# Kernel tuning notes

Measured on AMD Instinct MI355X. Metric: run time of the kernel, lower is better.

The kernel has to match this reference:

```python
import jax, jax.numpy as jnp
import numpy as np

ALPHA = 0.05   # propalpha
GDEP = 2       # gcn_depth
DIL = 2        # new_dilation
KSET = (2, 3, 6, 7)

def _dconv(x, w, b, d):
    # Conv2d(c_in, c_out, (1, k), dilation=(1, d), padding='same'), NCHW layout
    k = w.shape[-1]
    tot = d * (k - 1)
    lo = tot // 2
    y = jax.lax.conv_general_dilated(x, w, (1, 1), ((0, 0), (lo, tot - lo)),
                                     rhs_dilation=(1, d),
                                     dimension_numbers=('NCHW', 'OIHW', 'NCHW'))
    return y + b[None, :, None, None]

def _inception(x, ws, bs):
    # 'same' padding keeps seq_len for every branch, so the tail-slice is a no-op
    return jnp.concatenate([_dconv(x, w, b, DIL) for w, b in zip(ws, bs)], axis=1)

def _gcn(Hf, Aoff, W, b, n):
    # PyG GCNConv with unit edge weights (no edge_weight passed) and remaining self-loops:
    # out = D^-1/2 (A_off + I_R)^T D^-1/2 (Hf @ W^T) + b, where only rows < n carry edges.
    XW = Hf @ W.T
    deg = jnp.ones((Hf.shape[0],), Hf.dtype).at[:n].add(jnp.sum(Aoff, axis=0))
    dis = jax.lax.rsqrt(deg)
    out = XW / deg[:, None]                                           # self-loop term
    out = out.at[:n].add(dis[:n, None] * (Aoff.T @ (dis[:n, None] * XW[:n])))
    return out + b[None, :]

def _mixprop(X, A, gws, gbs, mw, mb):
    B, C, n, L = X.shape
    # dense_to_sparse ignores weights here (none passed to GCNConv) -> binary adjacency;
    # add_remaining_self_loops replaces any diagonal entries, so zero the diagonal.
    Aoff = (A != 0).astype(X.dtype) * (1.0 - jnp.eye(n, dtype=X.dtype))
    H = X
    hops = [X]
    for i in range(GDEP):
        Hf = H.reshape(B * L, C * n)   # torch row-major reshape, replicated exactly
        H1 = _gcn(Hf, Aoff, gws[i], gbs[i], n)
        H = ALPHA * X + H1.reshape(B, C, n, L)
        hops.append(H)
    Hc = jnp.concatenate(hops, axis=1)  # (B, (GDEP+1)*C, n, L)
    return jnp.einsum('bixl,oi->boxl', Hc, mw) + mb[None, :, None, None]

def _layernorm(x, w, b, idx, eps=1e-5):
    # F.layer_norm over all of x.shape[1:] with node-indexed affine params
    mu = jnp.mean(x, axis=(1, 2, 3), keepdims=True)
    var = jnp.var(x, axis=(1, 2, 3), keepdims=True)
    xh = (x - mu) * jax.lax.rsqrt(var + eps)
    return xh * w[:, idx, :][None] + b[:, idx, :][None]

def _forward(x, x_skip, A, idx, fws, fbs, gws, gbs, skip_w, skip_b,
             mp1_gw, mp1_gb, mp1_mw, mp1_mb, mp2_gw, mp2_gb, mp2_mw, mp2_mb,
             ln_w, ln_b):
    x_res = x
    xf = jnp.tanh(_inception(x, fws, fbs))
    xg = jax.nn.sigmoid(_inception(x, gws, gbs))
    x = xf * xg  # gated dilated temporal conv (dropout is an eval-mode no-op)
    x_skip = jnp.einsum('bixl,oi->boxl', x, skip_w) + skip_b[None, :, None, None] + x_skip
    x = (_mixprop(x, A, mp1_gw, mp1_gb, mp1_mw, mp1_mb)
         + _mixprop(x.swapaxes(0, 0), A.T, mp2_gw, mp2_gb, mp2_mw, mp2_mb))
    x = x + x_res[..., -x.shape[3]:]
    x = _layernorm(x, ln_w, ln_b, idx)
    return x, x_skip

def setup_inputs():
    key = jax.random.key(0)
    ks = jax.random.split(key, 32)
    B, C, N, L, SKIP = 16, 32, 128, 128, 64
    F = C * N
    co = C // len(KSET)
    d = {}
    d['x'] = jax.random.normal(ks[0], (B, C, N, L), jnp.float32)
    d['x_skip'] = jax.random.normal(ks[1], (B, SKIP, N, L), jnp.float32)
    d['A'] = jax.random.uniform(ks[2], (N, N), jnp.float32)
    d['idx'] = jnp.arange(N, dtype=jnp.int32)
    i = 3
    for pre in ('f', 'g'):
        for k in KSET:
            d[pre + 'w' + str(k)] = jax.random.normal(ks[i], (co, C, 1, k), jnp.float32) * float(1.0 / np.sqrt(C * k))
            d[pre + 'b' + str(k)] = jax.random.uniform(ks[i + 1], (co,), jnp.float32)
            i += 2
    d['skip_w'] = jax.random.normal(ks[i], (SKIP, C), jnp.float32) * float(1.0 / np.sqrt(C)); i += 1
    d['skip_b'] = jax.random.uniform(ks[i], (SKIP,), jnp.float32); i += 1
    for mp in ('mp1', 'mp2'):
        d[mp + '_gw'] = jax.random.normal(ks[i], (GDEP, F, F), jnp.float32) * float(1.0 / np.sqrt(F)); i += 1
        d[mp + '_gb'] = jnp.zeros((GDEP, F), jnp.float32)
        d[mp + '_mw'] = jax.random.normal(ks[i], (C, (GDEP + 1) * C), jnp.float32) * float(1.0 / np.sqrt((GDEP + 1) * C)); i += 1
        d[mp + '_mb'] = jax.random.uniform(ks[i], (C,), jnp.float32); i += 1
    d['ln_w'] = jnp.ones((C, N, L), jnp.float32)
    d['ln_b'] = jnp.zeros((C, N, L), jnp.float32)
    return d

def reference(x, x_skip, A, idx, fw2, fb2, fw3, fb3, fw6, fb6, fw7, fb7,
              gw2, gb2, gw3, gb3, gw6, gb6, gw7, gb7, skip_w, skip_b,
              mp1_gw, mp1_gb, mp1_mw, mp1_mb, mp2_gw, mp2_gb, mp2_mw, mp2_mb,
              ln_w, ln_b):
    return _forward(x, x_skip, A, idx,
                    [fw2, fw3, fw6, fw7], [fb2, fb3, fb6, fb7],
                    [gw2, gw3, gw6, gw7], [gb2, gb3, gb6, gb7],
                    skip_w, skip_b, mp1_gw, mp1_gb, mp1_mw, mp1_mb,
                    mp2_gw, mp2_gb, mp2_mw, mp2_mb, ln_w, ln_b)
```

## Files before the change

kernel.cpp:

```cpp
#include <hip/hip_runtime.h>
#include <stdint.h>

typedef unsigned short u16;
typedef unsigned int   u32;
typedef __attribute__((ext_vector_type(4))) float f32x4;
typedef __attribute__((ext_vector_type(8))) short bf16x8;

__device__ __forceinline__ u16 f2bf(float f) {
    u32 i = __float_as_uint(f);
    u32 r = (i + 0x7fffu + ((i >> 16) & 1u)) >> 16;
    return (u16)r;
}
__device__ __forceinline__ float bf2f(u16 u) {
    return __uint_as_float(((u32)u) << 16);
}
__device__ __forceinline__ u32 cvt2bf(float a, float b) {
    u32 r;
    asm("v_cvt_pk_bf16_f32 %0, %1, %2" : "=v"(r) : "v"(a), "v"(b));
    return r;
}

#define GLOAD16(g, l) __builtin_amdgcn_global_load_lds( \
    (const __attribute__((address_space(1))) void*)(g), \
    (__attribute__((address_space(3))) void*)(l), 16, 0, 0)

#define RAW_BARRIER()  asm volatile("s_barrier" ::: "memory")
#define VMCNT(n)       asm volatile("s_waitcnt vmcnt(" #n ")" ::: "memory")

__global__ __launch_bounds__(512, 1)
void k_gemm2g(const u16* __restrict__ A0, const u16* __restrict__ A1,
              const u16* __restrict__ B0, const u16* __restrict__ B1,
              const u16* __restrict__ Gres,
              const float* __restrict__ gb0, const float* __restrict__ gb1,
              u16* __restrict__ Ha, u16* __restrict__ Hb,
              float* __restrict__ XW0a, float* __restrict__ XW0b)
{
    __shared__ alignas(16) u16 LDS[65536];
    const int NT = 128;
    const int tid  = threadIdx.x;
    const int lane = tid & 63;
    const int wid  = tid >> 6;
    const int wr = wid >> 2, wc = wid & 3;

    const int bid = blockIdx.x;
    const int swz = (bid & 7) * 32 + (bid >> 3);
    const int z   = swz >> 7;
    const int rem = swz & 127;
    const int bm = (rem >> 4) * 256;
    const int bn = (rem & 15) * 256;

    const u16* Ap = (z ? A1 : A0) + (size_t)bm * 4096;
    const u16* Bp = (z ? B1 : B0) + (size_t)bn * 4096;

    int aoff[8], boff[4];
    #pragma unroll
    for (int i = 0; i < 8; ++i) {
        int row = wr * 128 + i * 16 + (lane & 15);
        int sp  = (lane >> 4) ^ ((row >> 1) & 3);
        aoff[i] = row * 32 + sp * 8;
    }
    #pragma unroll
    for (int j = 0; j < 4; ++j) {
        int row = wc * 64 + j * 16 + (lane & 15);
        int sp  = (lane >> 4) ^ ((row >> 1) & 3);
        boff[j] = row * 32 + sp * 8;
    }

    auto stage = [&](int t) {
        if (t >= NT) return;
        const int k0  = t << 5;
        u16* buf = LDS + ((t & 3) << 14);
        #pragma unroll
        for (int h = 0; h < 2; ++h) {
            const int c  = tid + h * 512;
            const int r  = c >> 2;
            const int sl = (c & 3) ^ ((r >> 1) & 3);
            GLOAD16(Ap + (size_t)r * 4096 + k0 + sl * 8, buf + c * 8);
            GLOAD16(Bp + (size_t)r * 4096 + k0 + sl * 8, buf + 8192 + c * 8);
        }
    };

    f32x4 acc[8][4] = {};

    auto compute = [&](int t) {
        const u16* buf = LDS + ((t & 3) << 14);
        bf16x8 af[8], bf[4];
        #pragma unroll
        for (int j = 0; j < 4; ++j) bf[j] = *(const bf16x8*)(buf + 8192 + boff[j]);
        #pragma unroll
        for (int i = 0; i < 8; ++i) af[i] = *(const bf16x8*)(buf + aoff[i]);
        __builtin_amdgcn_s_setprio(1);
        #pragma unroll
        for (int i = 0; i < 8; ++i)
            #pragma unroll
            for (int j = 0; j < 4; ++j)
                acc[i][j] = __builtin_amdgcn_mfma_f32_16x16x32_bf16(af[i], bf[j], acc[i][j], 0, 0, 0);
        __builtin_amdgcn_s_setprio(0);
    };

    stage(0); stage(1); stage(2);
    for (int t = 0; t < NT - 3; ++t) {
        VMCNT(8);
        RAW_BARRIER();
        stage(t + 3);
        compute(t);
    }
    VMCNT(8);  RAW_BARRIER(); compute(NT - 3);
    VMCNT(4);  RAW_BARRIER(); compute(NT - 2);
    VMCNT(0);  RAW_BARRIER(); compute(NT - 1);

    const int orow = (lane >> 4) * 4, ocol = lane & 15;
    const float* gbv = z ? gb1 : gb0;
    u16* H = z ? Hb : Ha;

    #pragma unroll
    for (int j = 0; j < 4; ++j) {
        const int o = bn + wc * 64 + j * 16 + ocol;
        const float gbo = gbv[o];
        #pragma unroll
        for (int i = 0; i < 8; ++i) {
            const int rbase = bm + wr * 128 + i * 16 + orow;
            #pragma unroll
            for (int v = 0; v < 4; ++v) {
                const size_t e = (size_t)(rbase + v) * 4096 + o;
                float g = bf2f(Gres[e]);
                H[e] = f2bf(__fmaf_rn(0.05f, g, acc[i][j][v] + gbo));
            }
        }
    }
    if (bm == 0 && wr == 0) {
        float* XW0 = z ? XW0b : XW0a;
        #pragma unroll
        for (int i = 0; i < 8; ++i) {
            #pragma unroll
            for (int j = 0; j < 4; ++j) {
                float* cp = XW0 + (size_t)(i * 16 + orow) * 4096 + (bn + wc * 64 + j * 16 + ocol);
                #pragma unroll
                for (int v = 0; v < 4; ++v)
                    cp[(size_t)v * 4096] = acc[i][j][v];
            }
        }
    }
}

__device__ __forceinline__ void wcvt_body(int wb, const float* __restrict__ W0,
                                          const float* __restrict__ W1,
                                          u16* __restrict__ Wb0, u16* __restrict__ Wb1)
{
    int half = wb >> 13;
    const float* W = half ? W1 : W0;
    u16* Wb = half ? Wb1 : Wb0;
    size_t e = ((size_t)(wb & 8191) * 256 + threadIdx.x) * 8;
    f32x4 a = *(const f32x4*)(W + e);
    f32x4 b = *(const f32x4*)(W + e + 4);
    uint4 r;
    r.x = cvt2bf(a[0], a[1]); r.y = cvt2bf(a[2], a[3]);
    r.z = cvt2bf(b[0], b[1]); r.w = cvt2bf(b[2], b[3]);
    *(uint4*)(Wb + e) = r;
}

__device__ __forceinline__ void prep_body(const float* __restrict__ A, float* dd)
{
    int r = threadIdx.x;
    if (r >= 128) return;
    int cc = 0, cr = 0;
    for (int j = 0; j < 128; ++j) {
        if (j == r) continue;
        if (A[(j << 7) + r] != 0.f) cc++;
        if (A[(r << 7) + j] != 0.f) cr++;
    }
    float d1 = 1.f + (float)cc, d2 = 1.f + (float)cr;
    dd[r]       = rsqrtf(d1); dd[128 + r] = 1.f / d1;
    dd[256 + r] = rsqrtf(d2); dd[384 + r] = 1.f / d2;
}

__device__ __forceinline__ void gcnfix_body(int fb, const float* __restrict__ XW0a,
              const float* __restrict__ XW0b,
              const u16* __restrict__ G, const float* __restrict__ Af,
              const float* __restrict__ dd,
              const float* __restrict__ gb0, const float* __restrict__ gb1,
              u16* __restrict__ Ha, u16* __restrict__ Hb)
{
    const int prob = fb >> 9;
    const int rem  = fb & 511;
    const int t4 = rem * 256 + threadIdx.x;
    const int r = t4 >> 10, og = (t4 & 1023) << 2;
    const float* XW0 = prob ? XW0b : XW0a;
    const float* dis = prob ? dd + 256 : dd;
    const float* inv = prob ? dd + 384 : dd + 128;
    const float* gb  = prob ? gb1  : gb0;
    u16* H = prob ? Hb : Ha;

    const size_t e = ((size_t)r << 12) + og;
    f32x4 xw = *(const f32x4*)(XW0 + e);
    f32x4 s = {0.f, 0.f, 0.f, 0.f};
    for (int j = 0; j < 128; ++j) {
        float av = prob ? Af[(r << 7) + j] : Af[(j << 7) + r];
        float wv = ((av != 0.f) && (j != r)) ? dis[j] : 0.f;
        f32x4 xv = *(const f32x4*)(XW0 + ((size_t)j << 12) + og);
        #pragma unroll
        for (int q = 0; q < 4; ++q) s[q] = __fmaf_rn(wv, xv[q], s[q]);
    }
    const float iv = inv[r], dr = dis[r];
    f32x4 gb4 = *(const f32x4*)(gb + og);
    uint2 gv = *(const uint2*)(G + e);
    float g0 = __uint_as_float(gv.x << 16), g1 = __uint_as_float(gv.x & 0xffff0000u);
    float g2 = __uint_as_float(gv.y << 16), g3 = __uint_as_float(gv.y & 0xffff0000u);
    float y0 = __fmaf_rn(0.05f, g0, __fmaf_rn(dr, s[0], xw[0] * iv) + gb4[0]);
    float y1 = __fmaf_rn(0.05f, g1, __fmaf_rn(dr, s[1], xw[1] * iv) + gb4[1]);
    float y2 = __fmaf_rn(0.05f, g2, __fmaf_rn(dr, s[2], xw[2] * iv) + gb4[2]);
    float y3 = __fmaf_rn(0.05f, g3, __fmaf_rn(dr, s[3], xw[3] * iv) + gb4[3]);
    uint2 rr;
    rr.x = cvt2bf(y0, y1);
    rr.y = cvt2bf(y2, y3);
    *(uint2*)(H + e) = rr;
}

__device__ __forceinline__ constexpr int wbase_of(int k) {
    return k == 2 ? 0 : k == 3 ? 520 : k == 6 ? 1296 : 2840;
}
__device__ __forceinline__ constexpr int ob_of(int k) {
    return k == 2 ? 0 : k == 3 ? 8 : k == 6 ? 16 : 24;
}

template<int KA, int KB>
__device__ __forceinline__ void conv_dual(const float* __restrict__ xsb,
                                          const float* __restrict__ wfA,
                                          const float* __restrict__ wgA,
                                          const float* __restrict__ wfB,
                                          const float* __restrict__ wgB,
                                          float fbA, float gbA, float fbB, float gbB,
                                          u16* __restrict__ GpA, u16* __restrict__ GpB,
                                          u16* __restrict__ GsA, u16* __restrict__ GsB)
{
    float afA[8], agA[8], afB[8], agB[8];
    #pragma unroll
    for (int i = 0; i < 8; ++i) {
        afA[i] = fbA; agA[i] = gbA;
        afB[i] = fbB; agB[i] = gbB;
    }
    for (int c = 0; c < 32; ++c) {
        float xw[24];
        const float* xr = xsb + c * 144;
        #pragma unroll
        for (int q = 0; q < 6; ++q) {
            f32x4 v = *(const f32x4*)(xr + q * 4);
            xw[q * 4 + 0] = v[0]; xw[q * 4 + 1] = v[1];
            xw[q * 4 + 2] = v[2]; xw[q * 4 + 3] = v[3];
        }
        {
            float wf[KA], wg[KA];
            const float* pf = wfA + c * KA;
            const float* pg = wgA + c * KA;
            #pragma unroll
            for (int j = 0; j < KA; ++j) { wf[j] = pf[j]; wg[j] = pg[j]; }
            #pragma unroll
            for (int li = 0; li < 8; ++li) {
                #pragma unroll
                for (int j = 0; j < KA; ++j) {
                    float xv = xw[li + 8 - (KA - 1) + 2 * j];
                    afA[li] = __fmaf_rn(xv, wf[j], afA[li]);
                    agA[li] = __fmaf_rn(xv, wg[j], agA[li]);
                }
            }
        }
        {
            float wf[KB], wg[KB];
            const float* pf = wfB + c * KB;
            const float* pg = wgB + c * KB;
            #pragma unroll
            for (int j = 0; j < KB; ++j) { wf[j] = pf[j]; wg[j] = pg[j]; }
            #pragma unroll
            for (int li = 0; li < 8; ++li) {
                #pragma unroll
                for (int j = 0; j < KB; ++j) {
                    float xv = xw[li + 8 - (KB - 1) + 2 * j];
                    afB[li] = __fmaf_rn(xv, wf[j], afB[li]);
                    agB[li] = __fmaf_rn(xv, wg[j], agB[li]);
                }
            }
        }
    }
    u16 oA[8], oB[8];
    #pragma unroll
    for (int i = 0; i < 8; ++i) {
        float e2 = __expf(2.f * afA[i]);
        float th = 1.f - __fdividef(2.f, e2 + 1.f);
        float sg = __fdividef(1.f, 1.f + __expf(-agA[i]));
        oA[i] = f2bf(th * sg);
        float e2b = __expf(2.f * afB[i]);
        float thb = 1.f - __fdividef(2.f, e2b + 1.f);
        float sgb = __fdividef(1.f, 1.f + __expf(-agB[i]));
        oB[i] = f2bf(thb * sgb);
    }
    uint4 uA, uB;
    uA.x = oA[0] | ((u32)oA[1] << 16); uA.y = oA[2] | ((u32)oA[3] << 16);
    uA.z = oA[4] | ((u32)oA[5] << 16); uA.w = oA[6] | ((u32)oA[7] << 16);
    uB.x = oB[0] | ((u32)oB[1] << 16); uB.y = oB[2] | ((u32)oB[3] << 16);
    uB.z = oB[4] | ((u32)oB[5] << 16); uB.w = oB[6] | ((u32)oB[7] << 16);
    *(uint4*)GpA = uA; *(uint4*)GpB = uB;
    *(uint4*)GsA = uA; *(uint4*)GsB = uB;
}

__global__ __launch_bounds__(256)
void k_mega1(const float* __restrict__ x,
             const float* __restrict__ fw2p, const float* __restrict__ fw3p,
             const float* __restrict__ fw6p, const float* __restrict__ fw7p,
             const float* __restrict__ fb2p, const float* __restrict__ fb3p,
             const float* __restrict__ fb6p, const float* __restrict__ fb7p,
             const float* __restrict__ gw2p, const float* __restrict__ gw3p,
             const float* __restrict__ gw6p, const float* __restrict__ gw7p,
             const float* __restrict__ gb2p, const float* __restrict__ gb3p,
             const float* __restrict__ gb6p, const float* __restrict__ gb7p,
             const float* __restrict__ sw,   const float* __restrict__ sb,
             const float* __restrict__ xskip,
             u16* __restrict__ G, float* __restrict__ outp,
             const float* __restrict__ W0, const float* __restrict__ W1,
             u16* __restrict__ Wb0, u16* __restrict__ Wb1,
             const float* __restrict__ A, float* __restrict__ dd)
{
    const int bid = blockIdx.x;
    if (bid >= 2048) {
        if (bid < 18432) wcvt_body(bid - 2048, W0, W1, Wb0, Wb1);
        else             prep_body(A, dd);
        return;
    }
    __shared__ alignas(16) float xs[32 * 144];
    __shared__ float wfl[4640], wgl[4640];
    __shared__ float fbl[32], gbl[32];
    __shared__ alignas(16) u16 Gs[4096];
    __shared__ float swl[64 * 33];
    __shared__ float sbl[64];
    const int tid = threadIdx.x;
    const int b = bid >> 7, n = bid & 127;

    for (int i = tid; i < 32 * 144; i += 256) xs[i] = 0.f;
    for (int g = tid; g < 4608; g += 256) {
        int rel, k, woff;
        const float *pf, *pg;
        if (g < 512)       { rel = g;        k = 2; woff = 0;    pf = fw2p; pg = gw2p; }
        else if (g < 1280) { rel = g - 512;  k = 3; woff = 520;  pf = fw3p; pg = gw3p; }
        else if (g < 2816) { rel = g - 1280; k = 6; woff = 1296; pf = fw6p; pg = gw6p; }
        else               { rel = g - 2816; k = 7; woff = 2840; pf = fw7p; pg = gw7p; }
        int ck = 32 * k;
        int oo = rel / ck, rem = rel % ck;
        int dst = woff + oo * (ck + 1) + rem;
        wfl[dst] = pf[rel];
        wgl[dst] = pg[rel];
    }
    for (int i = tid; i < 2048; i += 256) swl[(i >> 5) * 33 + (i & 31)] = sw[i];
    if (tid < 64) sbl[tid] = sb[tid];
    if (tid < 32) {
        int br = tid >> 3, oo = tid & 7;
        const float* pf = br == 0 ? fb2p : br == 1 ? fb3p : br == 2 ? fb6p : fb7p;
        const float* pg = br == 0 ? gb2p : br == 1 ? gb3p : br == 2 ? gb6p : gb7p;
        fbl[tid] = pf[oo]; gbl[tid] = pg[oo];
    }
    __syncthreads();
    const float* xb = x + (size_t)b * 524288 + n * 128;
    for (int p = 0; p < 4; ++p) {
        int chunk = p * 256 + tid;
        int c = chunk >> 5, l4 = (chunk & 31) * 4;
        *(f32x4*)&xs[c * 144 + 8 + l4] = *(const f32x4*)(xb + (size_t)c * 16384 + l4);
    }
    __syncthreads();

    {
        const int w = tid >> 6, lane = tid & 63;
        const int oo = lane >> 3, lL = lane & 7;
        const int h  = w & 1;
        const int l0 = h * 64 + lL * 8;
        const float* xsb = xs + l0;
        size_t gbase = ((size_t)b * 32 * 128 + n) * 128 + l0;
        if (w < 2) {
            constexpr int KA = 2, KB = 7;
            const int oA = ob_of(KA) + oo, oB = ob_of(KB) + oo;
            conv_dual<KA, KB>(xsb,
                wfl + wbase_of(KA) + oo * (32 * KA + 1), wgl + wbase_of(KA) + oo * (32 * KA + 1),
                wfl + wbase_of(KB) + oo * (32 * KB + 1), wgl + wbase_of(KB) + oo * (32 * KB + 1),
                fbl[oA], gbl[oA], fbl[oB], gbl[oB],
                G + gbase + (size_t)oA * 16384, G + gbase + (size_t)oB * 16384,
                Gs + oA * 128 + l0, Gs + oB * 128 + l0);
        } else {
            constexpr int KA = 3, KB = 6;
            const int oA = ob_of(KA) + oo, oB = ob_of(KB) + oo;
            conv_dual<KA, KB>(xsb,
                wfl + wbase_of(KA) + oo * (32 * KA + 1), wgl + wbase_of(KA) + oo * (32 * KA + 1),
                wfl + wbase_of(KB) + oo * (32 * KB + 1), wgl + wbase_of(KB) + oo * (32 * KB + 1),
                fbl[oA], gbl[oA], fbl[oB], gbl[oB],
                G + gbase + (size_t)oA * 16384, G + gbase + (size_t)oB * 16384,
                Gs + oA * 128 + l0, Gs + oB * 128 + l0);
        }
    }
    __syncthreads();

    const int sg = (tid & 15) * 4, l0s = (tid >> 4) * 8;
    float acc[4][8];
    #pragma unroll
    for (int si = 0; si < 4; ++si) {
        float bv = sbl[sg + si];
        #pragma unroll
        for (int li = 0; li < 8; ++li) acc[si][li] = bv;
    }
    for (int c = 0; c < 32; ++c) {
        uint4 gv = *(const uint4*)&Gs[c * 128 + l0s];
        float g[8];
        g[0] = __uint_as_float(gv.x << 16); g[1] = __uint_as_float(gv.x & 0xffff0000u);
        g[2] = __uint_as_float(gv.y << 16); g[3] = __uint_as_float(gv.y & 0xffff0000u);
        g[4] = __uint_as_float(gv.z << 16); g[5] = __uint_as_float(gv.z & 0xffff0000u);
        g[6] = __uint_as_float(gv.w << 16); g[7] = __uint_as_float(gv.w & 0xffff0000u);
        #pragma unroll
        for (int si = 0; si < 4; ++si) {
            float wv = swl[(sg + si) * 33 + c];
            #pragma unroll
            for (int li = 0; li < 8; ++li) acc[si][li] = __fmaf_rn(g[li], wv, acc[si][li]);
        }
    }
    #pragma unroll
    for (int si = 0; si < 4; ++si) {
        size_t e = ((size_t)(b * 64 + sg + si) * 128 + n) * 128 + l0s;
        f32x4 x0 = *(const f32x4*)(xskip + e);
        f32x4 x1 = *(const f32x4*)(xskip + e + 4);
        f32x4 r0, r1;
        r0[0] = acc[si][0] + x0[0]; r0[1] = acc[si][1] + x0[1];
        r0[2] = acc[si][2] + x0[2]; r0[3] = acc[si][3] + x0[3];
        r1[0] = acc[si][4] + x1[0]; r1[1] = acc[si][5] + x1[1];
        r1[2] = acc[si][6] + x1[2]; r1[3] = acc[si][7] + x1[3];
        *(f32x4*)(outp + e)     = r0;
        *(f32x4*)(outp + e + 4) = r1;
    }
}

__global__ __launch_bounds__(256)
void k_mega2(const float* __restrict__ XW0a, const float* __restrict__ XW0b,
             const u16* __restrict__ G, const float* __restrict__ Af,
             const float* __restrict__ dd,
             const float* __restrict__ gb0, const float* __restrict__ gb1,
             u16* __restrict__ Ha, u16* __restrict__ Hb,
             const float* __restrict__ W0, const float* __restrict__ W1,
             u16* __restrict__ Wb0, u16* __restrict__ Wb1)
{
    const int bid = blockIdx.x;
    if (bid < 1024) gcnfix_body(bid, XW0a, XW0b, G, Af, dd, gb0, gb1, Ha, Hb);
    else            wcvt_body(bid - 1024, W0, W1, Wb0, Wb1);
}

__global__ __launch_bounds__(256)
void k_gcnfix(const float* __restrict__ XW0a, const float* __restrict__ XW0b,
              const u16* __restrict__ G, const float* __restrict__ Af,
              const float* __restrict__ dd,
              const float* __restrict__ gb0, const float* __restrict__ gb1,
              u16* __restrict__ Ha, u16* __restrict__ Hb)
{
    gcnfix_body(blockIdx.x, XW0a, XW0b, G, Af, dd, gb0, gb1, Ha, Hb);
}

__global__ __launch_bounds__(256)
void k_mix2ln(const u16* __restrict__ G,
              const u16* __restrict__ H1, const u16* __restrict__ H2,
              const u16* __restrict__ H1b, const u16* __restrict__ H2b,
              const float* __restrict__ mw1, const float* __restrict__ mb1,
              const float* __restrict__ mw2, const float* __restrict__ mb2,
              const float* __restrict__ x,
              u16* __restrict__ Y, float* __restrict__ partial)
{
    __shared__ alignas(16) u16 Gs[4096], H1s[4096], H2s[4096], H1bs[4096], H2bs[4096];
    __shared__ float wSg[32 * 33], wS11[32 * 33], wS12[32 * 33], wS21[32 * 33], wS22[32 * 33];
    __shared__ float mbl[32];
    const int tid = threadIdx.x;
    const int b = blockIdx.x >> 7, xn = blockIdx.x & 127;
    size_t base = (size_t)b * 524288 + xn * 128;
    for (int p = 0; p < 2; ++p) {
        int chunk = p * 256 + tid, c = chunk >> 4, l8 = (chunk & 15) * 8;
        size_t src = base + (size_t)c * 16384 + l8;
        *(uint4*)&Gs[c * 128 + l8]   = *(const uint4*)(G + src);
        *(uint4*)&H1s[c * 128 + l8]  = *(const uint4*)(H1 + src);
        *(uint4*)&H2s[c * 128 + l8]  = *(const uint4*)(H2 + src);
        *(uint4*)&H1bs[c * 128 + l8] = *(const uint4*)(H1b + src);
        *(uint4*)&H2bs[c * 128 + l8] = *(const uint4*)(H2b + src);
    }
    for (int i = tid; i < 1024; i += 256) {
        int o = i >> 5, c = i & 31;
        int d = o * 33 + c;
        wSg[d]  = mw1[o * 96 + c] + mw2[o * 96 + c];
        wS11[d] = mw1[o * 96 + 32 + c];
        wS12[d] = mw1[o * 96 + 64 + c];
        wS21[d] = mw2[o * 96 + 32 + c];
        wS22[d] = mw2[o * 96 + 64 + c];
    }
    if (tid < 32) mbl[tid] = mb1[tid] + mb2[tid];
    __syncthreads();
    const int og = (tid & 7) * 4, l0 = (tid >> 3) * 4;
    float acc[4][4];
    #pragma unroll
    for (int oi = 0; oi < 4; ++oi) {
        float bv = mbl[og + oi];
        acc[oi][0] = bv; acc[oi][1] = bv; acc[oi][2] = bv; acc[oi][3] = bv;
    }
    for (int c = 0; c < 32; ++c) {
        uint2 ga = *(const uint2*)&Gs[c * 128 + l0];
        uint2 h1 = *(const uint2*)&H1s[c * 128 + l0];
        uint2 h2 = *(const uint2*)&H2s[c * 128 + l0];
        uint2 j1 = *(const uint2*)&H1bs[c * 128 + l0];
        uint2 j2 = *(const uint2*)&H2bs[c * 128 + l0];
        float gv[4], v1[4], v2[4], u1[4], u2[4];
        gv[0] = __uint_as_float(ga.x << 16); gv[1] = __uint_as_float(ga.x & 0xffff0000u);
        gv[2] = __uint_as_float(ga.y << 16); gv[3] = __uint_as_float(ga.y & 0xffff0000u);
        v1[0] = __uint_as_float(h1.x << 16); v1[1] = __uint_as_float(h1.x & 0xffff0000u);
        v1[2] = __uint_as_float(h1.y << 16); v1[3] = __uint_as_float(h1.y & 0xffff0000u);
        v2[0] = __uint_as_float(h2.x << 16); v2[1] = __uint_as_float(h2.x & 0xffff0000u);
        v2[2] = __uint_as_float(h2.y << 16); v2[3] = __uint_as_float(h2.y & 0xffff0000u);
        u1[0] = __uint_as_float(j1.x << 16); u1[1] = __uint_as_float(j1.x & 0xffff0000u);
        u1[2] = __uint_as_float(j1.y << 16); u1[3] = __uint_as_float(j1.y & 0xffff0000u);
        u2[0] = __uint_as_float(j2.x << 16); u2[1] = __uint_as_float(j2.x & 0xffff0000u);
        u2[2] = __uint_as_float(j2.y << 16); u2[3] = __uint_as_float(j2.y & 0xffff0000u);
        #pragma unroll
        for (int oi = 0; oi < 4; ++oi) {
            int d = (og + oi) * 33 + c;
            float a0 = wSg[d], a1 = wS11[d], a2 = wS12[d], a3 = wS21[d], a4 = wS22[d];
            #pragma unroll
            for (int li = 0; li < 4; ++li)
                acc[oi][li] += gv[li] * a0 + v1[li] * a1 + v2[li] * a2
                             + u1[li] * a3 + u2[li] * a4;
        }
    }
    float s = 0.f, ss = 0.f;
    #pragma unroll
    for (int oi = 0; oi < 4; ++oi) {
        size_t e = ((size_t)(b * 32 + og + oi) * 128 + xn) * 128 + l0;
        f32x4 xv = *(const f32x4*)(x + e);
        float y0 = acc[oi][0] + xv[0];
        float y1 = acc[oi][1] + xv[1];
        float y2 = acc[oi][2] + xv[2];
        float y3 = acc[oi][3] + xv[3];
        s  += y0 + y1 + y2 + y3;
        ss += y0 * y0 + y1 * y1 + y2 * y2 + y3 * y3;
        uint2 rr;
        rr.x = cvt2bf(y0, y1);
        rr.y = cvt2bf(y2, y3);
        *(uint2*)(Y + e) = rr;
    }
    #pragma unroll
    for (int o = 32; o > 0; o >>= 1) {
        s  += __shfl_down(s,  o, 64);
        ss += __shfl_down(ss, o, 64);
    }
    __shared__ float sred[8];
    int w = tid >> 6;
    if ((tid & 63) == 0) { sred[w * 2] = s; sred[w * 2 + 1] = ss; }
    __syncthreads();
    if (tid == 0) {
        partial[blockIdx.x * 2]     = sred[0] + sred[2] + sred[4] + sred[6];
        partial[blockIdx.x * 2 + 1] = sred[1] + sred[3] + sred[5] + sred[7];
    }
}

__global__ __launch_bounds__(256)
void k_lnnorm(const u16* __restrict__ Y,
              const float* __restrict__ partial, const int* __restrict__ idxp,
              const float* __restrict__ lnw, const float* __restrict__ lnb,
              float* __restrict__ outx)
{
    const int tid = threadIdx.x;
    const int b = blockIdx.x >> 7, chunk = blockIdx.x & 127;
    float s = 0.f, ss = 0.f;
    if (tid < 128) {
        s  = partial[(b * 128 + tid) * 2];
        ss = partial[(b * 128 + tid) * 2 + 1];
    }
    #pragma unroll
    for (int o = 32; o > 0; o >>= 1) {
        s  += __shfl_down(s,  o, 64);
        ss += __shfl_down(ss, o, 64);
    }
    __shared__ float sred[4];
    __shared__ float mv[2];
    if ((tid & 63) == 0 && tid < 128) { sred[(tid >> 6) * 2] = s; sred[(tid >> 6) * 2 + 1] = ss; }
    __syncthreads();
    if (tid == 0) {
        float S = sred[0] + sred[2], SS = sred[1] + sred[3];
        float mean = S * (1.f / 524288.f);
        float var = SS * (1.f / 524288.f) - mean * mean;
        mv[0] = mean; mv[1] = rsqrtf(var + 1e-5f);
    }
    __syncthreads();
    const float mean = mv[0], rstd = mv[1];
    #pragma unroll
    for (int q = 0; q < 4; ++q) {
        int ib = chunk * 4096 + q * 1024 + tid * 4;
        size_t e = (size_t)b * 524288 + ib;
        uint2 yv2 = *(const uint2*)(Y + e);
        float y[4];
        y[0] = __uint_as_float(yv2.x << 16); y[1] = __uint_as_float(yv2.x & 0xffff0000u);
        y[2] = __uint_as_float(yv2.y << 16); y[3] = __uint_as_float(yv2.y & 0xffff0000u);
        int c = ib >> 14, xn = (ib >> 7) & 127, l = ib & 127;
        int ix = idxp[xn];
        size_t we = ((size_t)c * 128 + ix) * 128 + l;
        f32x4 wv = *(const f32x4*)(lnw + we);
        f32x4 bv = *(const f32x4*)(lnb + we);
        f32x4 r;
        #pragma unroll
        for (int j = 0; j < 4; ++j)
            r[j] = (y[j] - mean) * rstd * wv[j] + bv[j];
        *(f32x4*)(outx + e) = r;
    }
}

extern "C" void kernel_launch(void* const* d_in, const int* in_sizes, int n_in,
                              void* d_out, int out_size, void* d_ws, size_t ws_size,
                              hipStream_t stream)
{
    (void)in_sizes; (void)n_in; (void)out_size; (void)ws_size;
    const float* x      = (const float*)d_in[0];
    const float* xskip  = (const float*)d_in[1];
    const float* A      = (const float*)d_in[2];
    const int*   idxp   = (const int*)d_in[3];
    const float* fw2p = (const float*)d_in[4];  const float* fb2p = (const float*)d_in[5];
    const float* fw3p = (const float*)d_in[6];  const float* fb3p = (const float*)d_in[7];
    const float* fw6p = (const float*)d_in[8];  const float* fb6p = (const float*)d_in[9];
    const float* fw7p = (const float*)d_in[10]; const float* fb7p = (const float*)d_in[11];
    const float* gw2p = (const float*)d_in[12]; const float* gb2p = (const float*)d_in[13];
    const float* gw3p = (const float*)d_in[14]; const float* gb3p = (const float*)d_in[15];
    const float* gw6p = (const float*)d_in[16]; const float* gb6p = (const float*)d_in[17];
    const float* gw7p = (const float*)d_in[18]; const float* gb7p = (const float*)d_in[19];
    const float* sw   = (const float*)d_in[20]; const float* sb   = (const float*)d_in[21];
    const float* mp1_gw = (const float*)d_in[22]; const float* mp1_gb = (const float*)d_in[23];
    const float* mp1_mw = (const float*)d_in[24]; const float* mp1_mb = (const float*)d_in[25];
    const float* mp2_gw = (const float*)d_in[26]; const float* mp2_gb = (const float*)d_in[27];
    const float* mp2_mw = (const float*)d_in[28]; const float* mp2_mb = (const float*)d_in[29];
    const float* lnw = (const float*)d_in[30]; const float* lnb = (const float*)d_in[31];

    char* wsb = (char*)d_ws;
    float* out_x  = (float*)d_out;
    float* out_sk = out_x + 8388608;

    const size_t MB16 = 16777216, MB33 = 33554432;
    u16*   G    = (u16*)(wsb);
    u16*   H1   = (u16*)(wsb + MB16);
    u16*   H1b  = (u16*)(wsb + 2 * MB16);
    u16*   H2   = (u16*)(wsb + 3 * MB16);
    u16*   H2b  = (u16*)(wsb + 4 * MB16);
    u16*   Wb0  = (u16*)(wsb + 5 * MB16);
    u16*   Wb1  = (u16*)(wsb + 5 * MB16 + MB33);
    u16*   Yb   = (u16*)Wb0;
    float* XW0a = (float*)(wsb + 5 * MB16 + 2 * MB33);
    float* XW0b = (float*)(wsb + 5 * MB16 + 2 * MB33 + 2097152);
    float* part = (float*)(wsb + 5 * MB16 + 2 * MB33 + 4194304);
    float* dd   = (float*)(wsb + 5 * MB16 + 2 * MB33 + 4194304 + 16384);

    k_mega1<<<18433, 256, 0, stream>>>(x, fw2p, fw3p, fw6p, fw7p, fb2p, fb3p, fb6p, fb7p,
                                       gw2p, gw3p, gw6p, gw7p, gb2p, gb3p, gb6p, gb7p,
                                       sw, sb, xskip, G, out_sk,
                                       mp1_gw, mp2_gw, Wb0, Wb1, A, dd);
    k_gemm2g<<<256, 512, 0, stream>>>(G, G, Wb0, Wb1, G, mp1_gb, mp2_gb,
                                      H1, H1b, XW0a, XW0b);
    k_mega2<<<17408, 256, 0, stream>>>(XW0a, XW0b, G, A, dd, mp1_gb, mp2_gb,
                                       H1, H1b, mp1_gw + MB16, mp2_gw + MB16, Wb0, Wb1);
    k_gemm2g<<<256, 512, 0, stream>>>(H1, H1b, Wb0, Wb1, G, mp1_gb + 4096, mp2_gb + 4096,
                                      H2, H2b, XW0a, XW0b);
    k_gcnfix<<<1024, 256, 0, stream>>>(XW0a, XW0b, G, A, dd,
                                       mp1_gb + 4096, mp2_gb + 4096, H2, H2b);
    k_mix2ln<<<2048, 256, 0, stream>>>(G, H1, H2, H1b, H2b, mp1_mw, mp1_mb,
                                       mp2_mw, mp2_mb, x, Yb, part);
    k_lnnorm<<<2048, 256, 0, stream>>>(Yb, part, idxp, lnw, lnb, out_x);
}
```

Measured before the change: 644.0 us.

## Split inception from weight-convert kernel and store conv weights as bf16 in LDS

The fused mega1 kernel is split into a standalone weight-conversion/prep kernel and a dedicated inception+skip kernel. Inside the inception kernel the filter and gate conv weights are stored in shared memory as bf16 instead of fp32, which halves that LDS footprint and should let more blocks fit per CU. The trade-off is an extra kernel launch, losing the overlap between conv blocks and conversion blocks, and reduced weight precision in the dilated convolutions.

```diff
diff --git a/kernel.cpp b/kernel.cpp
--- a/kernel.cpp
+++ b/kernel.cpp
@@ -216,6 +216,40 @@
     *(uint2*)(H + e) = rr;
 }
 
+__global__ __launch_bounds__(256)
+void k_wcvtprep(const float* __restrict__ W0, const float* __restrict__ W1,
+                u16* __restrict__ Wb0, u16* __restrict__ Wb1,
+                const float* __restrict__ A, float* __restrict__ dd)
+{
+    const int bid = blockIdx.x;
+    if (bid < 16384) wcvt_body(bid, W0, W1, Wb0, Wb1);
+    else             prep_body(A, dd);
+}
+
+__global__ __launch_bounds__(256)
+void k_mega2(const float* __restrict__ XW0a, const float* __restrict__ XW0b,
+             const u16* __restrict__ G, const float* __restrict__ Af,
+             const float* __restrict__ dd,
+             const float* __restrict__ gb0, const float* __restrict__ gb1,
+             u16* __restrict__ Ha, u16* __restrict__ Hb,
+             const float* __restrict__ W0, const float* __restrict__ W1,
+             u16* __restrict__ Wb0, u16* __restrict__ Wb1)
+{
+    const int bid = blockIdx.x;
+    if (bid < 1024) gcnfix_body(bid, XW0a, XW0b, G, Af, dd, gb0, gb1, Ha, Hb);
+    else            wcvt_body(bid - 1024, W0, W1, Wb0, Wb1);
+}
+
+__global__ __launch_bounds__(256)
+void k_gcnfix(const float* __restrict__ XW0a, const float* __restrict__ XW0b,
+              const u16* __restrict__ G, const float* __restrict__ Af,
+              const float* __restrict__ dd,
+              const float* __restrict__ gb0, const float* __restrict__ gb1,
+              u16* __restrict__ Ha, u16* __restrict__ Hb)
+{
+    gcnfix_body(blockIdx.x, XW0a, XW0b, G, Af, dd, gb0, gb1, Ha, Hb);
+}
+
 __device__ __forceinline__ constexpr int wbase_of(int k) {
     return k == 2 ? 0 : k == 3 ? 520 : k == 6 ? 1296 : 2840;
 }
@@ -225,10 +259,10 @@
 
 template<int KA, int KB>
 __device__ __forceinline__ void conv_dual(const float* __restrict__ xsb,
-                                          const float* __restrict__ wfA,
-                                          const float* __restrict__ wgA,
-                                          const float* __restrict__ wfB,
-                                          const float* __restrict__ wgB,
+                                          const u16* __restrict__ wfA,
+                                          const u16* __restrict__ wgA,
+                                          const u16* __restrict__ wfB,
+                                          const u16* __restrict__ wgB,
                                           float fbA, float gbA, float fbB, float gbB,
                                           u16* __restrict__ GpA, u16* __restrict__ GpB,
                                           u16* __restrict__ GsA, u16* __restrict__ GsB)
@@ -250,10 +284,10 @@
         }
         {
             float wf[KA], wg[KA];
-            const float* pf = wfA + c * KA;
-            const float* pg = wgA + c * KA;
-            #pragma unroll
-            for (int j = 0; j < KA; ++j) { wf[j] = pf[j]; wg[j] = pg[j]; }
+            const u16* pf = wfA + c * KA;
+            const u16* pg = wgA + c * KA;
+            #pragma unroll
+            for (int j = 0; j < KA; ++j) { wf[j] = bf2f(pf[j]); wg[j] = bf2f(pg[j]); }
             #pragma unroll
             for (int li = 0; li < 8; ++li) {
                 #pragma unroll
@@ -266,10 +300,10 @@
         }
         {
             float wf[KB], wg[KB];
-            const float* pf = wfB + c * KB;
-            const float* pg = wgB + c * KB;
-            #pragma unroll
-            for (int j = 0; j < KB; ++j) { wf[j] = pf[j]; wg[j] = pg[j]; }
+            const u16* pf = wfB + c * KB;
+            const u16* pg = wgB + c * KB;
+            #pragma unroll
+            for (int j = 0; j < KB; ++j) { wf[j] = bf2f(pf[j]); wg[j] = bf2f(pg[j]); }
             #pragma unroll
             for (int li = 0; li < 8; ++li) {
                 #pragma unroll
@@ -303,36 +337,27 @@
 }
 
 __global__ __launch_bounds__(256)
-void k_mega1(const float* __restrict__ x,
-             const float* __restrict__ fw2p, const float* __restrict__ fw3p,
-             const float* __restrict__ fw6p, const float* __restrict__ fw7p,
-             const float* __restrict__ fb2p, const float* __restrict__ fb3p,
-             const float* __restrict__ fb6p, const float* __restrict__ fb7p,
-             const float* __restrict__ gw2p, const float* __restrict__ gw3p,
-             const float* __restrict__ gw6p, const float* __restrict__ gw7p,
-             const float* __restrict__ gb2p, const float* __restrict__ gb3p,
-             const float* __restrict__ gb6p, const float* __restrict__ gb7p,
-             const float* __restrict__ sw,   const float* __restrict__ sb,
-             const float* __restrict__ xskip,
-             u16* __restrict__ G, float* __restrict__ outp,
-             const float* __restrict__ W0, const float* __restrict__ W1,
-             u16* __restrict__ Wb0, u16* __restrict__ Wb1,
-             const float* __restrict__ A, float* __restrict__ dd)
-{
-    const int bid = blockIdx.x;
-    if (bid >= 2048) {
-        if (bid < 18432) wcvt_body(bid - 2048, W0, W1, Wb0, Wb1);
-        else             prep_body(A, dd);
-        return;
-    }
+void k_incskip(const float* __restrict__ x,
+               const float* __restrict__ fw2p, const float* __restrict__ fw3p,
+               const float* __restrict__ fw6p, const float* __restrict__ fw7p,
+               const float* __restrict__ fb2p, const float* __restrict__ fb3p,
+               const float* __restrict__ fb6p, const float* __restrict__ fb7p,
+               const float* __restrict__ gw2p, const float* __restrict__ gw3p,
+               const float* __restrict__ gw6p, const float* __restrict__ gw7p,
+               const float* __restrict__ gb2p, const float* __restrict__ gb3p,
+               const float* __restrict__ gb6p, const float* __restrict__ gb7p,
+               const float* __restrict__ sw,   const float* __restrict__ sb,
+               const float* __restrict__ xskip,
+               u16* __restrict__ G, float* __restrict__ outp)
+{
     __shared__ alignas(16) float xs[32 * 144];
-    __shared__ float wfl[4640], wgl[4640];
+    __shared__ u16 wfl[4640], wgl[4640];
     __shared__ float fbl[32], gbl[32];
     __shared__ alignas(16) u16 Gs[4096];
     __shared__ float swl[64 * 33];
     __shared__ float sbl[64];
     const int tid = threadIdx.x;
-    const int b = bid >> 7, n = bid & 127;
+    const int b = blockIdx.x >> 7, n = blockIdx.x & 127;
 
     for (int i = tid; i < 32 * 144; i += 256) xs[i] = 0.f;
     for (int g = tid; g < 4608; g += 256) {
@@ -345,8 +370,8 @@
         int ck = 32 * k;
         int oo = rel / ck, rem = rel % ck;
         int dst = woff + oo * (ck + 1) + rem;
-        wfl[dst] = pf[rel];
-        wgl[dst] = pg[rel];
+        wfl[dst] = f2bf(pf[rel]);
+        wgl[dst] = f2bf(pg[rel]);
     }
     for (int i = tid; i < 2048; i += 256) swl[(i >> 5) * 33 + (i & 31)] = sw[i];
     if (tid < 64) sbl[tid] = sb[tid];
@@ -432,30 +457,6 @@
 }
 
 __global__ __launch_bounds__(256)
-void k_mega2(const float* __restrict__ XW0a, const float* __restrict__ XW0b,
-             const u16* __restrict__ G, const float* __restrict__ Af,
-             const float* __restrict__ dd,
-             const float* __restrict__ gb0, const float* __restrict__ gb1,
-             u16* __restrict__ Ha, u16* __restrict__ Hb,
-             const float* __restrict__ W0, const float* __restrict__ W1,
-             u16* __restrict__ Wb0, u16* __restrict__ Wb1)
-{
-    const int bid = blockIdx.x;
-    if (bid < 1024) gcnfix_body(bid, XW0a, XW0b, G, Af, dd, gb0, gb1, Ha, Hb);
-    else            wcvt_body(bid - 1024, W0, W1, Wb0, Wb1);
-}
-
-__global__ __launch_bounds__(256)
-void k_gcnfix(const float* __restrict__ XW0a, const float* __restrict__ XW0b,
-              const u16* __restrict__ G, const float* __restrict__ Af,
-              const float* __restrict__ dd,
-              const float* __restrict__ gb0, const float* __restrict__ gb1,
-              u16* __restrict__ Ha, u16* __restrict__ Hb)
-{
-    gcnfix_body(blockIdx.x, XW0a, XW0b, G, Af, dd, gb0, gb1, Ha, Hb);
-}
-
-__global__ __launch_bounds__(256)
 void k_mix2ln(const u16* __restrict__ G,
               const u16* __restrict__ H1, const u16* __restrict__ H2,
               const u16* __restrict__ H1b, const u16* __restrict__ H2b,
@@ -648,10 +649,10 @@
     float* part = (float*)(wsb + 5 * MB16 + 2 * MB33 + 4194304);
     float* dd   = (float*)(wsb + 5 * MB16 + 2 * MB33 + 4194304 + 16384);
 
-    k_mega1<<<18433, 256, 0, stream>>>(x, fw2p, fw3p, fw6p, fw7p, fb2p, fb3p, fb6p, fb7p,
-                                       gw2p, gw3p, gw6p, gw7p, gb2p, gb3p, gb6p, gb7p,
-                                       sw, sb, xskip, G, out_sk,
-                                       mp1_gw, mp2_gw, Wb0, Wb1, A, dd);
+    k_wcvtprep<<<16385, 256, 0, stream>>>(mp1_gw, mp2_gw, Wb0, Wb1, A, dd);
+    k_incskip<<<2048, 256, 0, stream>>>(x, fw2p, fw3p, fw6p, fw7p, fb2p, fb3p, fb6p, fb7p,
+                                        gw2p, gw3p, gw6p, gw7p, gb2p, gb3p, gb6p, gb7p,
+                                        sw, sb, xskip, G, out_sk);
     k_gemm2g<<<256, 512, 0, stream>>>(G, G, Wb0, Wb1, G, mp1_gb, mp2_gb,
                                       H1, H1b, XW0a, XW0b);
     k_mega2<<<17408, 256, 0, stream>>>(XW0a, XW0b, G, A, dd, mp1_gb, mp2_gb,
```

New measurement: 709.8 us. 1.1x slower.
